# Kernel tuning notes

Hardware: AMD Instinct MI355X
Metric: run time of the kernel (lower is better)

The kernel has to match this reference:

```python
import jax, jax.numpy as jnp
import numpy as np

HIDDEN = 32  # hard-coded in the module


def _lstm_cell(x, h, c, W_ih, W_hh, b_ih, b_hh):
    # torch.nn.LSTMCell: gates in order i, f, g, o
    gates = x @ W_ih.T + b_ih + h @ W_hh.T + b_hh
    i, f, g, o = jnp.split(gates, 4, axis=-1)
    c_new = jax.nn.sigmoid(f) * c + jax.nn.sigmoid(i) * jnp.tanh(g)
    h_new = jax.nn.sigmoid(o) * jnp.tanh(c_new)
    return h_new, c_new


def setup_inputs() -> dict:
    key = jax.random.key(0)
    ks = jax.random.split(key, 11)
    B, T, d, len_out = 256, 1024, 8, 10
    s = 0.05
    return {
        "input": jax.random.normal(ks[0], (B, T, d), dtype=jnp.float32),
        "W_ih1": jax.random.normal(ks[1], (4 * HIDDEN, d), dtype=jnp.float32) * s,
        "W_hh1": jax.random.normal(ks[2], (4 * HIDDEN, HIDDEN), dtype=jnp.float32) * s,
        "b_ih1": jax.random.normal(ks[3], (4 * HIDDEN,), dtype=jnp.float32) * s,
        "b_hh1": jax.random.normal(ks[4], (4 * HIDDEN,), dtype=jnp.float32) * s,
        "W_ih2": jax.random.normal(ks[5], (4 * HIDDEN, HIDDEN), dtype=jnp.float32) * s,
        "W_hh2": jax.random.normal(ks[6], (4 * HIDDEN, HIDDEN), dtype=jnp.float32) * s,
        "b_ih2": jax.random.normal(ks[7], (4 * HIDDEN,), dtype=jnp.float32) * s,
        "b_hh2": jax.random.normal(ks[8], (4 * HIDDEN,), dtype=jnp.float32) * s,
        "W_lin": jax.random.normal(ks[9], (d * len_out, HIDDEN), dtype=jnp.float32) * s,
        "b_lin": jax.random.normal(ks[10], (d * len_out,), dtype=jnp.float32) * s,
    }


def reference(input, W_ih1, W_hh1, b_ih1, b_hh1, W_ih2, W_hh2, b_ih2, b_hh2, W_lin, b_lin):
    B, T, d = input.shape
    len_out = W_lin.shape[0] // d

    def step(carry, x_t):
        h1, c1, h2, c2 = carry
        h1, c1 = _lstm_cell(x_t, h1, c1, W_ih1, W_hh1, b_ih1, b_hh1)
        h2, c2 = _lstm_cell(h1, h2, c2, W_ih2, W_hh2, b_ih2, b_hh2)
        out = h2 @ W_lin.T + b_lin  # [B, d*len_out]
        return (h1, c1, h2, c2), out

    z = jnp.zeros((B, HIDDEN), dtype=input.dtype)
    init = (z, z, z, z)
    xs = jnp.swapaxes(input, 0, 1)  # [T, B, d]
    _, outs = jax.lax.scan(step, init, xs)  # [T, B, d*len_out]
    outs = jnp.swapaxes(outs, 0, 1)  # [B, T, d*len_out]
    return outs.reshape(B, T, d, len_out)
```

## Files before the change

kernel.cpp:

```cpp
#include <hip/hip_runtime.h>

#define TT  1024
#define DIN 8

__device__ __forceinline__ float fsig(float x) {
    float e = __builtin_amdgcn_exp2f(-1.4426950408889634f * x);
    return __builtin_amdgcn_rcpf(1.0f + e);
}
__device__ __forceinline__ float ftanh_(float x) {
    float e = __builtin_amdgcn_exp2f(-2.8853900817779268f * x);
    return 2.0f * __builtin_amdgcn_rcpf(1.0f + e) - 1.0f;
}
template<int CTRL>
__device__ __forceinline__ float dppf(float v) {
    return __uint_as_float((unsigned)__builtin_amdgcn_update_dpp(
        0, (int)__float_as_uint(v), CTRL, 0xF, 0xF, true));
}

__global__ void __launch_bounds__(512, 2)
lstm_rec(const float* __restrict__ x,
         const float* __restrict__ Wih1, const float* __restrict__ Whh1,
         const float* __restrict__ bih1, const float* __restrict__ bhh1,
         const float* __restrict__ Wih2, const float* __restrict__ Whh2,
         const float* __restrict__ bih2, const float* __restrict__ bhh2,
         float* __restrict__ out)
{
    const int tid  = threadIdx.x;
    const int wv   = tid >> 6;
    const int l    = tid & 63;
    const int part = l & 1;
    const int g    = (l >> 1) & 3;
    const int ul   = l >> 3;
    const int b    = blockIdx.x;
    const bool isL1 = (wv < 4);
    const int  wu   = isL1 ? wv : (wv - 4);
    const int  unit = wu*8 + ul;
    const bool isg  = (g == 2);

    __shared__ float hb1[2][32];
    __shared__ float hb2[2][32];
    if (tid < 64)       ((float*)hb1)[tid]      = 0.f;
    else if (tid < 128) ((float*)hb2)[tid - 64] = 0.f;

    float wg[20];
    float wA[16], wB[16];
    float bias = 0.f;

    if (isL1) {
        const int R = g*32 + unit;
        const float* wsrc = Whh1 + R*32 + part*16;
#pragma unroll
        for (int qq = 0; qq < 4; ++qq) {
            float4 v = reinterpret_cast<const float4*>(wsrc)[qq];
            wg[4*qq]=v.x; wg[4*qq+1]=v.y; wg[4*qq+2]=v.z; wg[4*qq+3]=v.w;
        }
        float4 xv = *reinterpret_cast<const float4*>(Wih1 + R*DIN + part*4);
        wg[16]=xv.x; wg[17]=xv.y; wg[18]=xv.z; wg[19]=xv.w;
        if (!part) bias = bih1[R] + bhh1[R];
    } else {
        const int hs = g & 1;
        const int k2 = g >> 1;
        const int Re = (2*k2)*32 + unit;
        const int Ro = (2*k2+1)*32 + unit;
        const int Rw = g*32 + unit;
        const float* base = part ? Wih2 : Whh2;
#pragma unroll
        for (int qq = 0; qq < 4; ++qq) {
            float4 va = reinterpret_cast<const float4*>(base + Re*32 + hs*16)[qq];
            wA[4*qq]=va.x; wA[4*qq+1]=va.y; wA[4*qq+2]=va.z; wA[4*qq+3]=va.w;
            float4 vb = reinterpret_cast<const float4*>(base + Ro*32 + hs*16)[qq];
            wB[4*qq]=vb.x; wB[4*qq+1]=vb.y; wB[4*qq+2]=vb.z; wB[4*qq+3]=vb.w;
        }
        bias = bih2[Rw] + bhh2[Rw];
    }

    float c = 0.f;

    const float* __restrict__ xb = x   + (size_t)b * (TT*DIN);
    float* __restrict__ outb     = out + (size_t)b * (TT*80);

    float4 xcur;
    if (isL1) xcur = *reinterpret_cast<const float4*>(xb + part*4);
    int xoff = DIN;
    int o2   = 0;

    __syncthreads();

#pragma unroll 1
    for (int t = 0; t <= TT; ++t) {
        const int p0  = t & 1;
        const int pm1 = p0 ^ 1;

        if (isL1) {
            if (t < TT) {
                const float* hin = &hb1[pm1][part << 4];
                float a0 = bias, a1 = 0.f, a2 = 0.f, a3 = 0.f;
#pragma unroll
                for (int qq = 0; qq < 4; ++qq) {
                    float4 v = reinterpret_cast<const float4*>(hin)[qq];
                    a0 += wg[4*qq]  *v.x; a1 += wg[4*qq+1]*v.y;
                    a2 += wg[4*qq+2]*v.z; a3 += wg[4*qq+3]*v.w;
                }
                a0 += wg[16]*xcur.x; a1 += wg[17]*xcur.y;
                a2 += wg[18]*xcur.z; a3 += wg[19]*xcur.w;
                xcur = *reinterpret_cast<const float4*>(xb + xoff + part*4);
                xoff = (xoff + DIN > (TT-1)*DIN) ? (TT-1)*DIN : (xoff + DIN);

                float sum  = (a0 + a1) + (a2 + a3);
                float full = sum + dppf<0xB1>(sum);
                float u  = isg ? (full + full) : full;
                float S  = fsig(u);
                float av = isg ? (S + S - 1.0f) : S;
                float itg = dppf<0x114>(av) * av;
                float fv  = dppf<0x112>(av);
                c = fv * c + itg;
                float so  = dppf<0x102>(av);
                float hv  = so * ftanh_(c);
                if ((l & 7) == 4) hb1[p0][unit] = hv;
            }
        } else {
            if (t >= 1) {
                const int hs = g & 1;
                const float* hin = part ? &hb1[pm1][hs << 4] : &hb2[p0][hs << 4];
                float4 hv4[4];
#pragma unroll
                for (int qq = 0; qq < 4; ++qq)
                    hv4[qq] = reinterpret_cast<const float4*>(hin)[qq];
                float e0 = 0.f, e1 = 0.f, o0 = 0.f, o1 = 0.f;
#pragma unroll
                for (int qq = 0; qq < 4; ++qq) {
                    e0 += wA[4*qq]  *hv4[qq].x; e1 += wA[4*qq+1]*hv4[qq].y;
                    e0 += wA[4*qq+2]*hv4[qq].z; e1 += wA[4*qq+3]*hv4[qq].w;
                    o0 += wB[4*qq]  *hv4[qq].x; o1 += wB[4*qq+1]*hv4[qq].y;
                    o0 += wB[4*qq+2]*hv4[qq].z; o1 += wB[4*qq+3]*hv4[qq].w;
                }
                float accE = e0 + e1;
                float accO = o0 + o1;
                accE += dppf<0xB1>(accE);
                accO += dppf<0xB1>(accO);
                float stage = hs ? accE : accO;
                float recv  = dppf<0x4E>(stage);
                float own   = hs ? accO : accE;
                float full  = own + recv + bias;

                float u  = isg ? (full + full) : full;
                float S  = fsig(u);
                float av = isg ? (S + S - 1.0f) : S;
                float itg = dppf<0x114>(av) * av;
                float fv  = dppf<0x112>(av);
                c = fv * c + itg;
                float so  = dppf<0x102>(av);
                float hv  = so * ftanh_(c);
                if ((l & 7) == 4) {
                    hb2[pm1][unit] = hv;
                    outb[o2 + unit] = hv;
                }
                o2 += 80;
            }
        }

        __syncthreads();
    }
}

__global__ void __launch_bounds__(256, 4)
out_lin(const float* __restrict__ Wlin, const float* __restrict__ blin,
        float* __restrict__ out, int ntiles)
{
    __shared__ float wl[80][36];
    __shared__ float bl[80];
    __shared__ float ht[16][36];
    const int tid = threadIdx.x;

#pragma unroll 1
    for (int i = tid; i < 640; i += 256) {
        const int cc = i >> 3, qq = i & 7;
        float4 v = reinterpret_cast<const float4*>(Wlin)[i];
        *reinterpret_cast<float4*>(&wl[cc][qq*4]) = v;
    }
    if (tid < 80) bl[tid] = blin[tid];
    __syncthreads();

    const int row = tid >> 4;
    const int cl  = tid & 15;

#pragma unroll 1
    for (int tile = blockIdx.x; tile < ntiles; tile += gridDim.x) {
        const size_t base = (size_t)tile * 16;
        if (tid < 128) {
            const int r = tid >> 3, qq = tid & 7;
            float4 v = *reinterpret_cast<const float4*>(out + (base + r)*80 + qq*4);
            *reinterpret_cast<float4*>(&ht[r][qq*4]) = v;
        }
        __syncthreads();

        float hr[32];
#pragma unroll
        for (int j = 0; j < 8; ++j) {
            float4 v = *reinterpret_cast<const float4*>(&ht[row][j*4]);
            hr[4*j]=v.x; hr[4*j+1]=v.y; hr[4*j+2]=v.z; hr[4*j+3]=v.w;
        }
        float res[5];
#pragma unroll
        for (int cj = 0; cj < 5; ++cj) {
            const int cc = cl + 16*cj;
            float a0 = bl[cc], a1 = 0.f, a2 = 0.f, a3 = 0.f;
#pragma unroll
            for (int k = 0; k < 32; k += 4) {
                a0 += wl[cc][k]  *hr[k];   a1 += wl[cc][k+1]*hr[k+1];
                a2 += wl[cc][k+2]*hr[k+2]; a3 += wl[cc][k+3]*hr[k+3];
            }
            res[cj] = (a0 + a1) + (a2 + a3);
        }
        __syncthreads();
#pragma unroll
        for (int cj = 0; cj < 5; ++cj)
            out[(base + row)*80 + cl + 16*cj] = res[cj];
    }
}

extern "C" void kernel_launch(void* const* d_in, const int* in_sizes, int n_in,
                              void* d_out, int out_size, void* d_ws, size_t ws_size,
                              hipStream_t stream) {
    const float* x    = (const float*)d_in[0];
    const float* Wih1 = (const float*)d_in[1];
    const float* Whh1 = (const float*)d_in[2];
    const float* bih1 = (const float*)d_in[3];
    const float* bhh1 = (const float*)d_in[4];
    const float* Wih2 = (const float*)d_in[5];
    const float* Whh2 = (const float*)d_in[6];
    const float* bih2 = (const float*)d_in[7];
    const float* bhh2 = (const float*)d_in[8];
    const float* Wlin = (const float*)d_in[9];
    const float* blin = (const float*)d_in[10];

    const int B = in_sizes[0] / (TT * DIN);
    const int ntiles = (B * TT) / 16;

    hipLaunchKernelGGL(lstm_rec, dim3(B), dim3(512), 0, stream,
                       x, Wih1, Whh1, bih1, bhh1,
                       Wih2, Whh2, bih2, bhh2,
                       (float*)d_out);
    hipLaunchKernelGGL(out_lin, dim3(2048), dim3(256), 0, stream,
                       Wlin, blin, (float*)d_out, ntiles);
}
```

Before: 392.7 us.

## Remap LSTM lanes to split reduction dimension across 8 lanes per unit

Reassigns work so each hidden unit uses 8 lanes, with each lane owning a slice of the input/hidden dimension for all four gates. Partial sums are combined with a 3-step DPP butterfly instead of a 2-lane gate split followed by cross-gate DPP shuffles. Every lane now evaluates all four activations redundantly, which removes the gate-exchange shuffles but adds more transcendental work per lane. The __syncthreads is also replaced with an inline-asm lgkmcnt wait plus s_barrier, which does not wait on outstanding vector-memory operations.

```diff
diff --git a/kernel.cpp b/kernel.cpp
--- a/kernel.cpp
+++ b/kernel.cpp
@@ -15,6 +15,11 @@
 __device__ __forceinline__ float dppf(float v) {
     return __uint_as_float((unsigned)__builtin_amdgcn_update_dpp(
         0, (int)__float_as_uint(v), CTRL, 0xF, 0xF, true));
+}
+#define RED8(a)  { a += dppf<0x141>(a); a += dppf<0x1B>(a); a += dppf<0xB1>(a); }
+
+__device__ __forceinline__ void bar_lgkm() {
+    asm volatile("s_waitcnt lgkmcnt(0)\n\ts_barrier" ::: "memory");
 }
 
 __global__ void __launch_bounds__(512, 2)
@@ -25,53 +30,48 @@
          const float* __restrict__ bih2, const float* __restrict__ bhh2,
          float* __restrict__ out)
 {
-    const int tid  = threadIdx.x;
-    const int wv   = tid >> 6;
-    const int l    = tid & 63;
-    const int part = l & 1;
-    const int g    = (l >> 1) & 3;
-    const int ul   = l >> 3;
-    const int b    = blockIdx.x;
+    const int tid = threadIdx.x;
+    const int wv  = tid >> 6;
+    const int l   = tid & 63;
+    const int s   = l & 7;
+    const int gi  = l >> 3;
+    const int b   = blockIdx.x;
     const bool isL1 = (wv < 4);
     const int  wu   = isL1 ? wv : (wv - 4);
-    const int  unit = wu*8 + ul;
-    const bool isg  = (g == 2);
+    const int  unit = wu*8 + gi;
 
     __shared__ float hb1[2][32];
     __shared__ float hb2[2][32];
     if (tid < 64)       ((float*)hb1)[tid]      = 0.f;
     else if (tid < 128) ((float*)hb2)[tid - 64] = 0.f;
 
-    float wg[20];
-    float wA[16], wB[16];
-    float bias = 0.f;
-
+    float w[32];
+    float bi, bf, bg, bo;
     if (isL1) {
-        const int R = g*32 + unit;
-        const float* wsrc = Whh1 + R*32 + part*16;
-#pragma unroll
-        for (int qq = 0; qq < 4; ++qq) {
-            float4 v = reinterpret_cast<const float4*>(wsrc)[qq];
-            wg[4*qq]=v.x; wg[4*qq+1]=v.y; wg[4*qq+2]=v.z; wg[4*qq+3]=v.w;
-        }
-        float4 xv = *reinterpret_cast<const float4*>(Wih1 + R*DIN + part*4);
-        wg[16]=xv.x; wg[17]=xv.y; wg[18]=xv.z; wg[19]=xv.w;
-        if (!part) bias = bih1[R] + bhh1[R];
+#pragma unroll
+        for (int r = 0; r < 4; ++r) {
+            const int R = r*32 + unit;
+#pragma unroll
+            for (int j = 0; j < 4; ++j) w[r*4 + j] = Whh1[R*32 + s*4 + j];
+            w[16 + r] = Wih1[R*DIN + s];
+        }
+        bi = bih1[unit]      + bhh1[unit];
+        bf = bih1[32 + unit] + bhh1[32 + unit];
+        bg = bih1[64 + unit] + bhh1[64 + unit];
+        bo = bih1[96 + unit] + bhh1[96 + unit];
     } else {
-        const int hs = g & 1;
-        const int k2 = g >> 1;
-        const int Re = (2*k2)*32 + unit;
-        const int Ro = (2*k2+1)*32 + unit;
-        const int Rw = g*32 + unit;
-        const float* base = part ? Wih2 : Whh2;
-#pragma unroll
-        for (int qq = 0; qq < 4; ++qq) {
-            float4 va = reinterpret_cast<const float4*>(base + Re*32 + hs*16)[qq];
-            wA[4*qq]=va.x; wA[4*qq+1]=va.y; wA[4*qq+2]=va.z; wA[4*qq+3]=va.w;
-            float4 vb = reinterpret_cast<const float4*>(base + Ro*32 + hs*16)[qq];
-            wB[4*qq]=vb.x; wB[4*qq+1]=vb.y; wB[4*qq+2]=vb.z; wB[4*qq+3]=vb.w;
-        }
-        bias = bih2[Rw] + bhh2[Rw];
+        const float* Wb = (s < 4) ? Whh2 : Wih2;
+        const int co = (s & 3) * 8;
+#pragma unroll
+        for (int r = 0; r < 4; ++r) {
+            const int R = r*32 + unit;
+#pragma unroll
+            for (int j = 0; j < 8; ++j) w[r*8 + j] = Wb[R*32 + co + j];
+        }
+        bi = bih2[unit]      + bhh2[unit];
+        bf = bih2[32 + unit] + bhh2[32 + unit];
+        bg = bih2[64 + unit] + bhh2[64 + unit];
+        bo = bih2[96 + unit] + bhh2[96 + unit];
     }
 
     float c = 0.f;
@@ -79,12 +79,13 @@
     const float* __restrict__ xb = x   + (size_t)b * (TT*DIN);
     float* __restrict__ outb     = out + (size_t)b * (TT*80);
 
-    float4 xcur;
-    if (isL1) xcur = *reinterpret_cast<const float4*>(xb + part*4);
-    int xoff = DIN;
-    int o2   = 0;
-
-    __syncthreads();
+    float xcur = 0.f;
+    if (isL1) xcur = xb[s];
+    int xoff = DIN + s;
+    const int XMAX = (TT-1)*DIN + s;
+    int o2 = 0;
+
+    bar_lgkm();
 
 #pragma unroll 1
     for (int t = 0; t <= TT; ++t) {
@@ -93,65 +94,47 @@
 
         if (isL1) {
             if (t < TT) {
-                const float* hin = &hb1[pm1][part << 4];
-                float a0 = bias, a1 = 0.f, a2 = 0.f, a3 = 0.f;
-#pragma unroll
-                for (int qq = 0; qq < 4; ++qq) {
-                    float4 v = reinterpret_cast<const float4*>(hin)[qq];
-                    a0 += wg[4*qq]  *v.x; a1 += wg[4*qq+1]*v.y;
-                    a2 += wg[4*qq+2]*v.z; a3 += wg[4*qq+3]*v.w;
-                }
-                a0 += wg[16]*xcur.x; a1 += wg[17]*xcur.y;
-                a2 += wg[18]*xcur.z; a3 += wg[19]*xcur.w;
-                xcur = *reinterpret_cast<const float4*>(xb + xoff + part*4);
-                xoff = (xoff + DIN > (TT-1)*DIN) ? (TT-1)*DIN : (xoff + DIN);
-
-                float sum  = (a0 + a1) + (a2 + a3);
-                float full = sum + dppf<0xB1>(sum);
-                float u  = isg ? (full + full) : full;
-                float S  = fsig(u);
-                float av = isg ? (S + S - 1.0f) : S;
-                float itg = dppf<0x114>(av) * av;
-                float fv  = dppf<0x112>(av);
-                c = fv * c + itg;
-                float so  = dppf<0x102>(av);
-                float hv  = so * ftanh_(c);
-                if ((l & 7) == 4) hb1[p0][unit] = hv;
+                float4 h4 = *reinterpret_cast<const float4*>(&hb1[pm1][s*4]);
+                float ai = w[0] *h4.x + w[16]*xcur;
+                float af = w[4] *h4.x + w[17]*xcur;
+                float ag = w[8] *h4.x + w[18]*xcur;
+                float ao = w[12]*h4.x + w[19]*xcur;
+                ai += w[1]*h4.y;  af += w[5]*h4.y;  ag += w[9] *h4.y;  ao += w[13]*h4.y;
+                ai += w[2]*h4.z;  af += w[6]*h4.z;  ag += w[10]*h4.z;  ao += w[14]*h4.z;
+                ai += w[3]*h4.w;  af += w[7]*h4.w;  ag += w[11]*h4.w;  ao += w[15]*h4.w;
+                xcur = xb[xoff];
+                xoff = (xoff + DIN > XMAX) ? XMAX : (xoff + DIN);
+                RED8(ai); RED8(af); RED8(ag); RED8(ao);
+                float si = fsig(ai + bi);
+                float sf = fsig(af + bf);
+                float tg = ftanh_(ag + bg);
+                float so = fsig(ao + bo);
+                c = sf * c + si * tg;
+                float hv = so * ftanh_(c);
+                if (s == 0) hb1[p0][unit] = hv;
             }
         } else {
             if (t >= 1) {
-                const int hs = g & 1;
-                const float* hin = part ? &hb1[pm1][hs << 4] : &hb2[p0][hs << 4];
-                float4 hv4[4];
-#pragma unroll
-                for (int qq = 0; qq < 4; ++qq)
-                    hv4[qq] = reinterpret_cast<const float4*>(hin)[qq];
-                float e0 = 0.f, e1 = 0.f, o0 = 0.f, o1 = 0.f;
-#pragma unroll
-                for (int qq = 0; qq < 4; ++qq) {
-                    e0 += wA[4*qq]  *hv4[qq].x; e1 += wA[4*qq+1]*hv4[qq].y;
-                    e0 += wA[4*qq+2]*hv4[qq].z; e1 += wA[4*qq+3]*hv4[qq].w;
-                    o0 += wB[4*qq]  *hv4[qq].x; o1 += wB[4*qq+1]*hv4[qq].y;
-                    o0 += wB[4*qq+2]*hv4[qq].z; o1 += wB[4*qq+3]*hv4[qq].w;
-                }
-                float accE = e0 + e1;
-                float accO = o0 + o1;
-                accE += dppf<0xB1>(accE);
-                accO += dppf<0xB1>(accO);
-                float stage = hs ? accE : accO;
-                float recv  = dppf<0x4E>(stage);
-                float own   = hs ? accO : accE;
-                float full  = own + recv + bias;
-
-                float u  = isg ? (full + full) : full;
-                float S  = fsig(u);
-                float av = isg ? (S + S - 1.0f) : S;
-                float itg = dppf<0x114>(av) * av;
-                float fv  = dppf<0x112>(av);
-                c = fv * c + itg;
-                float so  = dppf<0x102>(av);
-                float hv  = so * ftanh_(c);
-                if ((l & 7) == 4) {
+                const float* hin = (s < 4) ? &hb2[p0][(s & 3) * 8]
+                                           : &hb1[pm1][(s & 3) * 8];
+                float4 u0 = reinterpret_cast<const float4*>(hin)[0];
+                float4 u1 = reinterpret_cast<const float4*>(hin)[1];
+                float ai = w[0] *u0.x, af = w[8] *u0.x, ag = w[16]*u0.x, ao = w[24]*u0.x;
+                ai += w[1]*u0.y;  af += w[9] *u0.y;  ag += w[17]*u0.y;  ao += w[25]*u0.y;
+                ai += w[2]*u0.z;  af += w[10]*u0.z;  ag += w[18]*u0.z;  ao += w[26]*u0.z;
+                ai += w[3]*u0.w;  af += w[11]*u0.w;  ag += w[19]*u0.w;  ao += w[27]*u0.w;
+                ai += w[4]*u1.x;  af += w[12]*u1.x;  ag += w[20]*u1.x;  ao += w[28]*u1.x;
+                ai += w[5]*u1.y;  af += w[13]*u1.y;  ag += w[21]*u1.y;  ao += w[29]*u1.y;
+                ai += w[6]*u1.z;  af += w[14]*u1.z;  ag += w[22]*u1.z;  ao += w[30]*u1.z;
+                ai += w[7]*u1.w;  af += w[15]*u1.w;  ag += w[23]*u1.w;  ao += w[31]*u1.w;
+                RED8(ai); RED8(af); RED8(ag); RED8(ao);
+                float si = fsig(ai + bi);
+                float sf = fsig(af + bf);
+                float tg = ftanh_(ag + bg);
+                float so = fsig(ao + bo);
+                c = sf * c + si * tg;
+                float hv = so * ftanh_(c);
+                if (s == 0) {
                     hb2[pm1][unit] = hv;
                     outb[o2 + unit] = hv;
                 }
@@ -159,7 +142,7 @@
             }
         }
 
-        __syncthreads();
+        bar_lgkm();
     }
 }
 
```

Measured after the change: 425.0 us. +8.2%, slower.
